# Optimization experiments

Measured on AMD Instinct MI355X. Metric: run time of the kernel, lower is better.

The kernel has to match this reference:

```python
import jax, jax.numpy as jnp
import numpy as np

MAX_JOINTS = 143

def setup_inputs() -> dict:
    key = jax.random.key(0)
    ks = jax.random.split(key, 8)
    d_model, latent_dim, feat = 256, 512, 13
    s = lambda n: 1.0 / np.sqrt(n)
    return {
        "z": jax.random.normal(ks[0], (32, latent_dim), jnp.float32),
        "W_latent": jax.random.normal(ks[1], (latent_dim, d_model), jnp.float32) * s(latent_dim),
        "b_latent": jnp.zeros((d_model,), jnp.float32),
        "joint_emb": jax.random.normal(ks[2], (MAX_JOINTS, d_model), jnp.float32),
        "frame_emb": jax.random.normal(ks[3], (120, d_model), jnp.float32),
        "ln_gamma": jnp.ones((d_model,), jnp.float32),
        "ln_beta": jnp.zeros((d_model,), jnp.float32),
        "W1": jax.random.normal(ks[4], (d_model, d_model), jnp.float32) * s(d_model),
        "b1": jnp.zeros((d_model,), jnp.float32),
        "W2": jax.random.normal(ks[5], (d_model, feat), jnp.float32) * s(d_model),
        "b2": jnp.zeros((feat,), jnp.float32),
        "max_frames": 120,
    }

def reference(z, W_latent, b_latent, joint_emb, frame_emb, ln_gamma, ln_beta, W1, b1, W2, b2, max_frames):
    # base: [B, d]
    base = z @ W_latent + b_latent
    fe = frame_emb[:max_frames]  # [F, d]
    # three-way broadcast sum -> [B, J, F, d]
    hidden = base[:, None, None, :] + joint_emb[None, :, None, :] + fe[None, None, :, :]
    # LayerNorm over last dim (eps=1e-5, torch default)
    mu = jnp.mean(hidden, axis=-1, keepdims=True)
    var = jnp.mean(jnp.square(hidden - mu), axis=-1, keepdims=True)
    h = (hidden - mu) * jax.lax.rsqrt(var + 1e-5) * ln_gamma + ln_beta
    # MLP: Linear -> exact GELU -> Linear
    h = jax.nn.gelu(h @ W1 + b1, approximate=False)
    out = h @ W2 + b2  # [B, J, F, feat]
    return jnp.transpose(out, (0, 1, 3, 2))  # [B, J, feat, F]
```

## Files before the change

kernel.cpp:

```cpp
#include <hip/hip_runtime.h>
#include <hip/hip_bf16.h>

typedef __bf16 bf16x8 __attribute__((ext_vector_type(8)));
typedef float  f32x4  __attribute__((ext_vector_type(4)));
typedef float  f32x2  __attribute__((ext_vector_type(2)));

#define B_  32
#define J_  143
#define F_  120
#define D_  256
#define L_  512
#define C_  13
#define M_  4576
#define NK  256
#define QB  9
#define GRIDC 509
#define CLS 260
#define PXS 388

static __device__ __forceinline__ unsigned short bits(__bf16 h) {
  return __builtin_bit_cast(unsigned short, h);
}

__global__ __launch_bounds__(256) void prep_kernel(
    const float* __restrict__ z, const float* __restrict__ Wl,
    const float* __restrict__ bl, const float* __restrict__ W1,
    const float* __restrict__ gamma, const float* __restrict__ beta,
    const float* __restrict__ b1, const float* __restrict__ fe,
    const float* __restrict__ W2,
    float* __restrict__ base, unsigned short* __restrict__ BT,
    float* __restrict__ bW1, float* __restrict__ Sfe, float* __restrict__ Sfe2,
    unsigned short* __restrict__ W2T, float* __restrict__ P2f) {
  const int t = threadIdx.x, bid = blockIdx.x;
  const int lane = t & 63, wv = t >> 6;
  __shared__ float zs[L_];
  __shared__ float ra[4], rb[4];
  __shared__ float fegl[256], gl2[256];

  if (bid < 32) {
    zs[t]       = z[bid * L_ + t];
    zs[t + 256] = z[bid * L_ + t + 256];
    __syncthreads();
    float acc = 0.f;
    #pragma unroll 32
    for (int k = 0; k < L_; ++k) acc = __builtin_fmaf(zs[k], Wl[k * D_ + t], acc);
    base[bid * D_ + t] = acc + bl[t];
    return;
  }
  if (bid < 432) {
    const int n = bid - 32;
    if (n < 256) {
      const float w1v = W1[t * D_ + n];
      float a = gamma[t] * w1v;
      float b = beta[t] * w1v;
      const float wg = a;
      #pragma unroll
      for (int m = 1; m < 64; m <<= 1) { a += __shfl_xor(a, m); b += __shfl_xor(b, m); }
      if (lane == 0) { ra[wv] = a; rb[wv] = b; }
      __syncthreads();
      const float cs = ra[0] + ra[1] + ra[2] + ra[3];
      if (t == 0) bW1[n] = rb[0] + rb[1] + rb[2] + rb[3] + b1[n];
      const float m = __builtin_fmaf(cs, -1.f / 256.f, wg);
      BT[n * NK + t] = bits((__bf16)m);
    } else if (n < 376) {
      const int f = n - 256;
      const float v = fe[f * D_ + t];
      float a = v, b = v * v;
      #pragma unroll
      for (int m = 1; m < 64; m <<= 1) { a += __shfl_xor(a, m); b += __shfl_xor(b, m); }
      if (lane == 0) { ra[wv] = a; rb[wv] = b; }
      __syncthreads();
      if (t == 0) {
        Sfe[f]  = ra[0] + ra[1] + ra[2] + ra[3];
        Sfe2[f] = rb[0] + rb[1] + rb[2] + rb[3];
      }
      BT[n * NK + t] = bits((__bf16)v);
    } else if (n < 384) {
      BT[n * NK + t] = 0;
    } else {
      const int c = n - 384;
      const float v = (c < C_) ? W2[t * C_ + c] : 0.f;
      W2T[c * D_ + t] = bits((__bf16)v);
    }
    return;
  }
  {
    const int f = bid - 432;
    const float fv = fe[f * D_ + t];
    const float gv = gamma[t];
    fegl[t] = fv * gv;
    gl2[t]  = gv;
    float a = fv;
    #pragma unroll
    for (int m = 1; m < 64; m <<= 1) a += __shfl_xor(a, m);
    if (lane == 0) ra[wv] = a;
    __syncthreads();
    const float sfe = ra[0] + ra[1] + ra[2] + ra[3];
    float acc1 = 0.f, acc2 = 0.f;
    #pragma unroll 8
    for (int k = 0; k < 256; ++k) {
      const float w = W1[k * D_ + t];
      acc1 = __builtin_fmaf(fegl[k], w, acc1);
      acc2 = __builtin_fmaf(gl2[k],  w, acc2);
    }
    P2f[f * D_ + t] = __builtin_fmaf(-sfe * (1.f / 256.f), acc2, acc1);
  }
}

__global__ __launch_bounds__(512, 4) void megaC_kernel(
    const float* __restrict__ base, const float* __restrict__ joint,
    const unsigned short* __restrict__ BT, const float* __restrict__ P2f,
    const float* __restrict__ bW1,
    const float* __restrict__ Sfe, const float* __restrict__ Sfe2,
    const unsigned short* __restrict__ W2T, const float* __restrict__ b2,
    float* __restrict__ out) {
  __shared__ float cl[16 * CLS];
  __shared__ float px[QB * PXS];
  __shared__ float bw[256];
  __shared__ float rstdl[QB][128];
  __shared__ float Scl[QB], Sc2l[QB];
  __shared__ __align__(16) unsigned short w2l[4096];

  const int tid  = threadIdx.x;
  const int lane = tid & 63, wv = tid >> 6;
  const int lrow = lane & 15, lgrp = lane >> 4;
  const int bj0  = blockIdx.x * QB;

  #pragma unroll
  for (int i = 0; i < 8; ++i) {
    const int idx = tid + i * 512;
    const int row = idx >> 8, col = idx & 255;
    float v = 0.f;
    if (row < QB) {
      const int bj = min(bj0 + row, M_ - 1);
      const int b = bj / J_, j = bj - b * J_;
      v = base[b * D_ + col] + joint[j * D_ + col];
    }
    cl[row * CLS + col] = v;
  }
  if (tid < 256) {
    bw[tid] = bW1[tid];
    const int rr = tid >> 4;
    const int b0 = tid * 32;
    const int sb = b0 ^ ((rr & 7) << 4);
    *(uint4*)((char*)w2l + sb)        = *(const uint4*)((const char*)W2T + b0);
    *(uint4*)((char*)w2l + (sb ^ 16)) = *(const uint4*)((const char*)W2T + b0 + 16);
  }
  __syncthreads();

  for (int r = wv; r < QB; r += 8) {
    const float4 v4 = *(const float4*)(cl + r * CLS + lane * 4);
    float s = v4.x + v4.y + v4.z + v4.w;
    float q = __builtin_fmaf(v4.x, v4.x,
              __builtin_fmaf(v4.y, v4.y,
              __builtin_fmaf(v4.z, v4.z, v4.w * v4.w)));
    #pragma unroll
    for (int m = 1; m < 64; m <<= 1) { s += __shfl_xor(s, m); q += __shfl_xor(q, m); }
    if (lane == 0) { Scl[r] = s; Sc2l[r] = q; }
  }

  {
    const int colbase = wv * 48;
    f32x4 acc[3] = {};
    #pragma unroll
    for (int s8 = 0; s8 < 8; ++s8) {
      const int k0 = s8 * 32 + lgrp * 8;
      const float4 c0 = *(const float4*)(cl + lrow * CLS + k0);
      const float4 c1 = *(const float4*)(cl + lrow * CLS + k0 + 4);
      const float cc[8] = {c0.x, c0.y, c0.z, c0.w, c1.x, c1.y, c1.z, c1.w};
      bf16x8 ahi;
      #pragma unroll
      for (int e = 0; e < 8; ++e) ahi[e] = (__bf16)cc[e];
      bf16x8 bhi[3];
      #pragma unroll
      for (int cf = 0; cf < 3; ++cf)
        bhi[cf] = *(const bf16x8*)(BT + (size_t)(colbase + cf * 16 + lrow) * NK +
                                   lgrp * 8 + s8 * 32);
      #pragma unroll
      for (int cf = 0; cf < 3; ++cf)
        acc[cf] = __builtin_amdgcn_mfma_f32_16x16x32_bf16(ahi, bhi[cf], acc[cf], 0, 0, 0);
    }
    #pragma unroll
    for (int cf = 0; cf < 3; ++cf)
      #pragma unroll
      for (int r4 = 0; r4 < 4; ++r4) {
        const int row = lgrp * 4 + r4;
        if (row < QB)
          px[row * PXS + colbase + cf * 16 + lrow] = acc[cf][r4];
      }
  }
  __syncthreads();

  #pragma unroll
  for (int i = 0; i < 3; ++i) {
    const int id2 = tid + i * 512;
    if (id2 < QB * 128) {
      const int q = id2 >> 7;
      const int fr = id2 & 127;
      const int fc = fr < F_ ? fr : F_ - 1;
      const float X = px[q * PXS + 256 + fc];
      const float mu = (Scl[q] + Sfe[fc]) * (1.f / 256.f);
      const float ms = __builtin_fmaf(2.f, X, Sc2l[q] + Sfe2[fc]) * (1.f / 256.f);
      rstdl[q][fr] = rsqrtf(ms - mu * mu + 1e-5f);
    }
  }
  __syncthreads();

  const int r0 = wv * 16 + lrow;
  const int f0 = r0 < F_ ? r0 : F_ - 1;
  float rs[QB];
  #pragma unroll
  for (int q = 0; q < QB; ++q) rs[q] = rstdl[q][r0];
  const float* __restrict__ q0p = P2f + f0 * D_ + lgrp * 8;

  f32x4 acc2[QB] = {};
  #pragma unroll
  for (int s = 0; s < 8; ++s) {
    const int n0 = s * 32 + lgrp * 8;
    const float4 qa0 = *(const float4*)(q0p + s * 32);
    const float4 qa1 = *(const float4*)(q0p + s * 32 + 4);
    const bf16x8 w2f = *(const bf16x8*)((const char*)w2l +
        ((lrow * 512 + n0 * 2) ^ ((lrow & 7) << 4)));
    f32x2 QV[4], BV[4];
    QV[0].x = qa0.x; QV[0].y = qa0.y;
    QV[1].x = qa0.z; QV[1].y = qa0.w;
    QV[2].x = qa1.x; QV[2].y = qa1.y;
    QV[3].x = qa1.z; QV[3].y = qa1.w;
    #pragma unroll
    for (int ep = 0; ep < 4; ++ep) BV[ep] = *(const f32x2*)(&bw[n0 + 2 * ep]);

    #pragma unroll
    for (int g = 0; g < QB; g += 3) {
      f32x2 U[12];
      #pragma unroll
      for (int qq = 0; qq < 3; ++qq) {
        f32x2 RS; RS.x = rs[g + qq]; RS.y = rs[g + qq];
        #pragma unroll
        for (int ep = 0; ep < 4; ++ep) {
          const f32x2 P = *(const f32x2*)(&px[(g + qq) * PXS + n0 + 2 * ep]);
          U[qq * 4 + ep] = __builtin_elementwise_fma(RS, P + QV[ep], BV[ep]);
        }
      }
      f32x2 E[12];
      #pragma unroll
      for (int i = 0; i < 12; ++i) {
        const f32x2 u = U[i];
        const f32x2 x2 = u * u;
        const f32x2 tt = u * (x2 * -0.1029432f + -2.3022082f);
        E[i].x = __builtin_amdgcn_exp2f(tt.x);
        E[i].y = __builtin_amdgcn_exp2f(tt.y);
      }
      bf16x8 af[3];
      #pragma unroll
      for (int i = 0; i < 12; ++i) {
        const f32x2 d = E[i] + 1.0f;
        f32x2 r;
        r.x = __builtin_amdgcn_rcpf(d.x);
        r.y = __builtin_amdgcn_rcpf(d.y);
        const f32x2 G = U[i] * r;
        af[i >> 2][(i & 3) * 2]     = (__bf16)G.x;
        af[i >> 2][(i & 3) * 2 + 1] = (__bf16)G.y;
      }
      #pragma unroll
      for (int qq = 0; qq < 3; ++qq)
        acc2[g + qq] =
            __builtin_amdgcn_mfma_f32_16x16x32_bf16(af[qq], w2f, acc2[g + qq], 0, 0, 0);
    }
  }

  if (lrow < C_) {
    const float bias = b2[lrow];
    const int f = wv * 16 + lgrp * 4;
    if (f < F_) {
      #pragma unroll
      for (int q = 0; q < QB; ++q) {
        if (bj0 + q < M_) {
          float4 v;
          v.x = acc2[q][0] + bias;
          v.y = acc2[q][1] + bias;
          v.z = acc2[q][2] + bias;
          v.w = acc2[q][3] + bias;
          *(float4*)(out + (size_t)(bj0 + q) * (C_ * F_) + lrow * F_ + f) = v;
        }
      }
    }
  }
}

extern "C" void kernel_launch(void* const* d_in, const int* in_sizes, int n_in,
                              void* d_out, int out_size, void* d_ws, size_t ws_size,
                              hipStream_t stream) {
  const float* z     = (const float*)d_in[0];
  const float* Wl    = (const float*)d_in[1];
  const float* bl    = (const float*)d_in[2];
  const float* joint = (const float*)d_in[3];
  const float* fe    = (const float*)d_in[4];
  const float* gamma = (const float*)d_in[5];
  const float* beta  = (const float*)d_in[6];
  const float* W1    = (const float*)d_in[7];
  const float* b1    = (const float*)d_in[8];
  const float* W2    = (const float*)d_in[9];
  const float* b2    = (const float*)d_in[10];
  float* out = (float*)d_out;

  char* ws = (char*)d_ws;
  float*          base  = (float*)(ws + 0);
  unsigned short* W2T   = (unsigned short*)(ws + 32768);
  float*          bW1   = (float*)(ws + 40960);
  float*          Sfe   = (float*)(ws + 41984);
  float*          Sfe2  = (float*)(ws + 42496);
  float*          P2f   = (float*)(ws + 65536);
  unsigned short* BT    = (unsigned short*)(ws + 262144);

  prep_kernel<<<552, 256, 0, stream>>>(z, Wl, bl, W1, gamma, beta, b1, fe, W2,
                                       base, BT, bW1, Sfe, Sfe2, W2T, P2f);
  megaC_kernel<<<GRIDC, 512, 0, stream>>>(base, joint, BT, P2f, bW1,
                                          Sfe, Sfe2, W2T, b2, out);
}
```

Measured before the change: 69.00 us.

## Split fused kernel into standalone bf16 GEMM pass plus smaller-tile MLP kernel

Moves the first projection (base+joint rows times BT) and the per-row sum and sum-of-squares out of the main kernel into a separate tiled MFMA GEMM kernel that writes an intermediate PXg buffer to workspace. The main kernel then loads precomputed rows, processes 6 rows per block instead of 9 with higher occupancy (launch bounds 512,6), and no longer pays for redundant 16-row MFMA tiles where only 9 rows are used. This trades an extra launch and a global round-trip of the intermediate for better compute utilisation and occupancy. A runtime check on spill bytes falls back to the old fused kernel.

```diff
diff --git a/kernel.cpp b/kernel.cpp
--- a/kernel.cpp
+++ b/kernel.cpp
@@ -12,11 +12,11 @@
 #define L_  512
 #define C_  13
 #define M_  4576
+#define MPAD 4736
 #define NK  256
-#define QB  9
-#define GRIDC 509
 #define CLS 260
 #define PXS 388
+#define PXG 384
 
 static __device__ __forceinline__ unsigned short bits(__bf16 h) {
   return __builtin_bit_cast(unsigned short, h);
@@ -107,36 +107,91 @@
   }
 }
 
-__global__ __launch_bounds__(512, 4) void megaC_kernel(
+__global__ __launch_bounds__(256, 4) void gemmBk_kernel(
     const float* __restrict__ base, const float* __restrict__ joint,
-    const unsigned short* __restrict__ BT, const float* __restrict__ P2f,
+    const unsigned short* __restrict__ BT,
+    float* __restrict__ PXg, float* __restrict__ Sc, float* __restrict__ Sc2) {
+  const int tid = threadIdx.x, lane = tid & 63, wave = tid >> 6;
+  const int lrow = lane & 15, lgrp = lane >> 4;
+  const int rb_ = blockIdx.x / 6, cb_ = blockIdx.x % 6;
+  const int rowbase = rb_ * 64 + wave * 16;
+  const int colbase = cb_ * 64;
+  const int r = rowbase + lrow;
+  const int bj = min(r, M_ - 1);
+  const int b = bj / J_, j = bj - b * J_;
+  const float* p1 = base + b * D_;
+  const float* p2 = joint + j * D_;
+
+  f32x4 acc[4] = {};
+  float ssum = 0.f, ssq = 0.f;
+  #pragma unroll
+  for (int s8 = 0; s8 < 8; ++s8) {
+    const int k0 = s8 * 32 + lgrp * 8;
+    const float4 ca = *(const float4*)(p1 + k0);
+    const float4 cb4 = *(const float4*)(p1 + k0 + 4);
+    const float4 da = *(const float4*)(p2 + k0);
+    const float4 db = *(const float4*)(p2 + k0 + 4);
+    const float c[8] = {ca.x + da.x, ca.y + da.y, ca.z + da.z, ca.w + da.w,
+                        cb4.x + db.x, cb4.y + db.y, cb4.z + db.z, cb4.w + db.w};
+    bf16x8 ahi;
+    #pragma unroll
+    for (int e = 0; e < 8; ++e) ahi[e] = (__bf16)c[e];
+    if (cb_ == 0) {
+      #pragma unroll
+      for (int e = 0; e < 8; ++e) { ssum += c[e]; ssq = __builtin_fmaf(c[e], c[e], ssq); }
+    }
+    bf16x8 bhi[4];
+    #pragma unroll
+    for (int nf = 0; nf < 4; ++nf)
+      bhi[nf] = *(const bf16x8*)(BT + (size_t)(colbase + nf * 16 + lrow) * NK +
+                                 lgrp * 8 + s8 * 32);
+    #pragma unroll
+    for (int nf = 0; nf < 4; ++nf)
+      acc[nf] = __builtin_amdgcn_mfma_f32_16x16x32_bf16(ahi, bhi[nf], acc[nf], 0, 0, 0);
+  }
+
+  if (cb_ == 0) {
+    ssum += __shfl_xor(ssum, 16); ssum += __shfl_xor(ssum, 32);
+    ssq  += __shfl_xor(ssq, 16);  ssq  += __shfl_xor(ssq, 32);
+    if (lgrp == 0 && r < M_) { Sc[r] = ssum; Sc2[r] = ssq; }
+  }
+
+  #pragma unroll
+  for (int nf = 0; nf < 4; ++nf)
+    #pragma unroll
+    for (int r4 = 0; r4 < 4; ++r4)
+      PXg[(size_t)(rowbase + lgrp * 4 + r4) * PXG + colbase + nf * 16 + lrow] =
+          acc[nf][r4];
+}
+
+#define QB2 6
+#define GRIDC2 763
+__global__ __launch_bounds__(512, 6) void mainC2_kernel(
+    const float* __restrict__ PXg, const float* __restrict__ P2f,
     const float* __restrict__ bW1,
+    const float* __restrict__ Sc, const float* __restrict__ Sc2,
     const float* __restrict__ Sfe, const float* __restrict__ Sfe2,
     const unsigned short* __restrict__ W2T, const float* __restrict__ b2,
     float* __restrict__ out) {
-  __shared__ float cl[16 * CLS];
-  __shared__ float px[QB * PXS];
+  __shared__ float pxl[QB2 * PXS];
   __shared__ float bw[256];
-  __shared__ float rstdl[QB][128];
-  __shared__ float Scl[QB], Sc2l[QB];
+  __shared__ float rstdl[QB2][128];
+  __shared__ float Scl[QB2], Sc2l[QB2];
   __shared__ __align__(16) unsigned short w2l[4096];
 
   const int tid  = threadIdx.x;
   const int lane = tid & 63, wv = tid >> 6;
   const int lrow = lane & 15, lgrp = lane >> 4;
-  const int bj0  = blockIdx.x * QB;
-
-  #pragma unroll
-  for (int i = 0; i < 8; ++i) {
+  const int bj0  = blockIdx.x * QB2;
+
+  #pragma unroll
+  for (int i = 0; i < 5; ++i) {
     const int idx = tid + i * 512;
-    const int row = idx >> 8, col = idx & 255;
-    float v = 0.f;
-    if (row < QB) {
-      const int bj = min(bj0 + row, M_ - 1);
-      const int b = bj / J_, j = bj - b * J_;
-      v = base[b * D_ + col] + joint[j * D_ + col];
-    }
-    cl[row * CLS + col] = v;
+    if (idx < QB2 * PXG) {
+      const int q = idx / PXG;
+      const int n = idx - q * PXG;
+      pxl[q * PXS + n] = PXg[(size_t)(bj0 + q) * PXG + n];
+    }
   }
   if (tid < 256) {
     bw[tid] = bW1[tid];
@@ -146,59 +201,21 @@
     *(uint4*)((char*)w2l + sb)        = *(const uint4*)((const char*)W2T + b0);
     *(uint4*)((char*)w2l + (sb ^ 16)) = *(const uint4*)((const char*)W2T + b0 + 16);
   }
+  if (tid < QB2) {
+    const int bj = min(bj0 + tid, M_ - 1);
+    Scl[tid] = Sc[bj];
+    Sc2l[tid] = Sc2[bj];
+  }
   __syncthreads();
 
-  for (int r = wv; r < QB; r += 8) {
-    const float4 v4 = *(const float4*)(cl + r * CLS + lane * 4);
-    float s = v4.x + v4.y + v4.z + v4.w;
-    float q = __builtin_fmaf(v4.x, v4.x,
-              __builtin_fmaf(v4.y, v4.y,
-              __builtin_fmaf(v4.z, v4.z, v4.w * v4.w)));
-    #pragma unroll
-    for (int m = 1; m < 64; m <<= 1) { s += __shfl_xor(s, m); q += __shfl_xor(q, m); }
-    if (lane == 0) { Scl[r] = s; Sc2l[r] = q; }
-  }
-
-  {
-    const int colbase = wv * 48;
-    f32x4 acc[3] = {};
-    #pragma unroll
-    for (int s8 = 0; s8 < 8; ++s8) {
-      const int k0 = s8 * 32 + lgrp * 8;
-      const float4 c0 = *(const float4*)(cl + lrow * CLS + k0);
-      const float4 c1 = *(const float4*)(cl + lrow * CLS + k0 + 4);
-      const float cc[8] = {c0.x, c0.y, c0.z, c0.w, c1.x, c1.y, c1.z, c1.w};
-      bf16x8 ahi;
-      #pragma unroll
-      for (int e = 0; e < 8; ++e) ahi[e] = (__bf16)cc[e];
-      bf16x8 bhi[3];
-      #pragma unroll
-      for (int cf = 0; cf < 3; ++cf)
-        bhi[cf] = *(const bf16x8*)(BT + (size_t)(colbase + cf * 16 + lrow) * NK +
-                                   lgrp * 8 + s8 * 32);
-      #pragma unroll
-      for (int cf = 0; cf < 3; ++cf)
-        acc[cf] = __builtin_amdgcn_mfma_f32_16x16x32_bf16(ahi, bhi[cf], acc[cf], 0, 0, 0);
-    }
-    #pragma unroll
-    for (int cf = 0; cf < 3; ++cf)
-      #pragma unroll
-      for (int r4 = 0; r4 < 4; ++r4) {
-        const int row = lgrp * 4 + r4;
-        if (row < QB)
-          px[row * PXS + colbase + cf * 16 + lrow] = acc[cf][r4];
-      }
-  }
-  __syncthreads();
-
-  #pragma unroll
-  for (int i = 0; i < 3; ++i) {
+  #pragma unroll
+  for (int i = 0; i < 2; ++i) {
     const int id2 = tid + i * 512;
-    if (id2 < QB * 128) {
+    if (id2 < QB2 * 128) {
       const int q = id2 >> 7;
       const int fr = id2 & 127;
       const int fc = fr < F_ ? fr : F_ - 1;
-      const float X = px[q * PXS + 256 + fc];
+      const float X = pxl[q * PXS + 256 + fc];
       const float mu = (Scl[q] + Sfe[fc]) * (1.f / 256.f);
       const float ms = __builtin_fmaf(2.f, X, Sc2l[q] + Sfe2[fc]) * (1.f / 256.f);
       rstdl[q][fr] = rsqrtf(ms - mu * mu + 1e-5f);
@@ -208,12 +225,12 @@
 
   const int r0 = wv * 16 + lrow;
   const int f0 = r0 < F_ ? r0 : F_ - 1;
-  float rs[QB];
-  #pragma unroll
-  for (int q = 0; q < QB; ++q) rs[q] = rstdl[q][r0];
+  float rs[QB2];
+  #pragma unroll
+  for (int q = 0; q < QB2; ++q) rs[q] = rstdl[q][r0];
   const float* __restrict__ q0p = P2f + f0 * D_ + lgrp * 8;
 
-  f32x4 acc2[QB] = {};
+  f32x4 acc2[QB2] = {};
   #pragma unroll
   for (int s = 0; s < 8; ++s) {
     const int n0 = s * 32 + lgrp * 8;
@@ -230,7 +247,183 @@
     for (int ep = 0; ep < 4; ++ep) BV[ep] = *(const f32x2*)(&bw[n0 + 2 * ep]);
 
     #pragma unroll
-    for (int g = 0; g < QB; g += 3) {
+    for (int q = 0; q < QB2; ++q) {
+      f32x2 RS; RS.x = rs[q]; RS.y = rs[q];
+      f32x2 U[4];
+      #pragma unroll
+      for (int ep = 0; ep < 4; ++ep) {
+        const f32x2 P = *(const f32x2*)(&pxl[q * PXS + n0 + 2 * ep]);
+        U[ep] = __builtin_elementwise_fma(RS, P + QV[ep], BV[ep]);
+      }
+      f32x2 E[4];
+      #pragma unroll
+      for (int i = 0; i < 4; ++i) {
+        const f32x2 u = U[i];
+        const f32x2 x2 = u * u;
+        const f32x2 tt = u * (x2 * -0.1029432f + -2.3022082f);
+        E[i].x = __builtin_amdgcn_exp2f(tt.x);
+        E[i].y = __builtin_amdgcn_exp2f(tt.y);
+      }
+      bf16x8 af;
+      #pragma unroll
+      for (int i = 0; i < 4; ++i) {
+        const f32x2 d = E[i] + 1.0f;
+        f32x2 r;
+        r.x = __builtin_amdgcn_rcpf(d.x);
+        r.y = __builtin_amdgcn_rcpf(d.y);
+        const f32x2 G = U[i] * r;
+        af[i * 2]     = (__bf16)G.x;
+        af[i * 2 + 1] = (__bf16)G.y;
+      }
+      acc2[q] = __builtin_amdgcn_mfma_f32_16x16x32_bf16(af, w2f, acc2[q], 0, 0, 0);
+    }
+  }
+
+  if (lrow < C_) {
+    const float bias = b2[lrow];
+    const int f = wv * 16 + lgrp * 4;
+    if (f < F_) {
+      #pragma unroll
+      for (int q = 0; q < QB2; ++q) {
+        if (bj0 + q < M_) {
+          float4 v;
+          v.x = acc2[q][0] + bias;
+          v.y = acc2[q][1] + bias;
+          v.z = acc2[q][2] + bias;
+          v.w = acc2[q][3] + bias;
+          *(float4*)(out + (size_t)(bj0 + q) * (C_ * F_) + lrow * F_ + f) = v;
+        }
+      }
+    }
+  }
+}
+
+#define QB9 9
+#define GRIDC9 509
+__global__ __launch_bounds__(512, 4) void megaC_kernel(
+    const float* __restrict__ base, const float* __restrict__ joint,
+    const unsigned short* __restrict__ BT, const float* __restrict__ P2f,
+    const float* __restrict__ bW1,
+    const float* __restrict__ Sfe, const float* __restrict__ Sfe2,
+    const unsigned short* __restrict__ W2T, const float* __restrict__ b2,
+    float* __restrict__ out) {
+  __shared__ float cl[16 * CLS];
+  __shared__ float px[QB9 * PXS];
+  __shared__ float bw[256];
+  __shared__ float rstdl[QB9][128];
+  __shared__ float Scl[QB9], Sc2l[QB9];
+  __shared__ __align__(16) unsigned short w2l[4096];
+
+  const int tid  = threadIdx.x;
+  const int lane = tid & 63, wv = tid >> 6;
+  const int lrow = lane & 15, lgrp = lane >> 4;
+  const int bj0  = blockIdx.x * QB9;
+
+  #pragma unroll
+  for (int i = 0; i < 8; ++i) {
+    const int idx = tid + i * 512;
+    const int row = idx >> 8, col = idx & 255;
+    float v = 0.f;
+    if (row < QB9) {
+      const int bj = min(bj0 + row, M_ - 1);
+      const int b = bj / J_, j = bj - b * J_;
+      v = base[b * D_ + col] + joint[j * D_ + col];
+    }
+    cl[row * CLS + col] = v;
+  }
+  if (tid < 256) {
+    bw[tid] = bW1[tid];
+    const int rr = tid >> 4;
+    const int b0 = tid * 32;
+    const int sb = b0 ^ ((rr & 7) << 4);
+    *(uint4*)((char*)w2l + sb)        = *(const uint4*)((const char*)W2T + b0);
+    *(uint4*)((char*)w2l + (sb ^ 16)) = *(const uint4*)((const char*)W2T + b0 + 16);
+  }
+  __syncthreads();
+
+  for (int r = wv; r < QB9; r += 8) {
+    const float4 v4 = *(const float4*)(cl + r * CLS + lane * 4);
+    float s = v4.x + v4.y + v4.z + v4.w;
+    float q = __builtin_fmaf(v4.x, v4.x,
+              __builtin_fmaf(v4.y, v4.y,
+              __builtin_fmaf(v4.z, v4.z, v4.w * v4.w)));
+    #pragma unroll
+    for (int m = 1; m < 64; m <<= 1) { s += __shfl_xor(s, m); q += __shfl_xor(q, m); }
+    if (lane == 0) { Scl[r] = s; Sc2l[r] = q; }
+  }
+
+  {
+    const int colbase = wv * 48;
+    f32x4 acc[3] = {};
+    #pragma unroll
+    for (int s8 = 0; s8 < 8; ++s8) {
+      const int k0 = s8 * 32 + lgrp * 8;
+      const float4 c0 = *(const float4*)(cl + lrow * CLS + k0);
+      const float4 c1 = *(const float4*)(cl + lrow * CLS + k0 + 4);
+      const float cc[8] = {c0.x, c0.y, c0.z, c0.w, c1.x, c1.y, c1.z, c1.w};
+      bf16x8 ahi;
+      #pragma unroll
+      for (int e = 0; e < 8; ++e) ahi[e] = (__bf16)cc[e];
+      bf16x8 bhi[3];
+      #pragma unroll
+      for (int cf = 0; cf < 3; ++cf)
+        bhi[cf] = *(const bf16x8*)(BT + (size_t)(colbase + cf * 16 + lrow) * NK +
+                                   lgrp * 8 + s8 * 32);
+      #pragma unroll
+      for (int cf = 0; cf < 3; ++cf)
+        acc[cf] = __builtin_amdgcn_mfma_f32_16x16x32_bf16(ahi, bhi[cf], acc[cf], 0, 0, 0);
+    }
+    #pragma unroll
+    for (int cf = 0; cf < 3; ++cf)
+      #pragma unroll
+      for (int r4 = 0; r4 < 4; ++r4) {
+        const int row = lgrp * 4 + r4;
+        if (row < QB9)
+          px[row * PXS + colbase + cf * 16 + lrow] = acc[cf][r4];
+      }
+  }
+  __syncthreads();
+
+  #pragma unroll
+  for (int i = 0; i < 3; ++i) {
+    const int id2 = tid + i * 512;
+    if (id2 < QB9 * 128) {
+      const int q = id2 >> 7;
+      const int fr = id2 & 127;
+      const int fc = fr < F_ ? fr : F_ - 1;
+      const float X = px[q * PXS + 256 + fc];
+      const float mu = (Scl[q] + Sfe[fc]) * (1.f / 256.f);
+      const float ms = __builtin_fmaf(2.f, X, Sc2l[q] + Sfe2[fc]) * (1.f / 256.f);
+      rstdl[q][fr] = rsqrtf(ms - mu * mu + 1e-5f);
+    }
+  }
+  __syncthreads();
+
+  const int r0 = wv * 16 + lrow;
+  const int f0 = r0 < F_ ? r0 : F_ - 1;
+  float rs[QB9];
+  #pragma unroll
+  for (int q = 0; q < QB9; ++q) rs[q] = rstdl[q][r0];
+  const float* __restrict__ q0p = P2f + f0 * D_ + lgrp * 8;
+
+  f32x4 acc2[QB9] = {};
+  #pragma unroll
+  for (int s = 0; s < 8; ++s) {
+    const int n0 = s * 32 + lgrp * 8;
+    const float4 qa0 = *(const float4*)(q0p + s * 32);
+    const float4 qa1 = *(const float4*)(q0p + s * 32 + 4);
+    const bf16x8 w2f = *(const bf16x8*)((const char*)w2l +
+        ((lrow * 512 + n0 * 2) ^ ((lrow & 7) << 4)));
+    f32x2 QV[4], BV[4];
+    QV[0].x = qa0.x; QV[0].y = qa0.y;
+    QV[1].x = qa0.z; QV[1].y = qa0.w;
+    QV[2].x = qa1.x; QV[2].y = qa1.y;
+    QV[3].x = qa1.z; QV[3].y = qa1.w;
+    #pragma unroll
+    for (int ep = 0; ep < 4; ++ep) BV[ep] = *(const f32x2*)(&bw[n0 + 2 * ep]);
+
+    #pragma unroll
+    for (int g = 0; g < QB9; g += 3) {
       f32x2 U[12];
       #pragma unroll
       for (int qq = 0; qq < 3; ++qq) {
@@ -273,7 +466,7 @@
     const int f = wv * 16 + lgrp * 4;
     if (f < F_) {
       #pragma unroll
-      for (int q = 0; q < QB; ++q) {
+      for (int q = 0; q < QB9; ++q) {
         if (bj0 + q < M_) {
           float4 v;
           v.x = acc2[q][0] + bias;
@@ -309,11 +502,25 @@
   float*          bW1   = (float*)(ws + 40960);
   float*          Sfe   = (float*)(ws + 41984);
   float*          Sfe2  = (float*)(ws + 42496);
-  float*          P2f   = (float*)(ws + 65536);
+  float*          Sc    = (float*)(ws + 49152);
+  float*          Sc2   = (float*)(ws + 69632);
+  float*          P2f   = (float*)(ws + 98304);
   unsigned short* BT    = (unsigned short*)(ws + 262144);
+  float*          PXg   = (float*)(ws + 524288);
 
   prep_kernel<<<552, 256, 0, stream>>>(z, Wl, bl, W1, gamma, beta, b1, fe, W2,
                                        base, BT, bW1, Sfe, Sfe2, W2T, P2f);
-  megaC_kernel<<<GRIDC, 512, 0, stream>>>(base, joint, BT, P2f, bW1,
-                                          Sfe, Sfe2, W2T, b2, out);
+
+  hipFuncAttributes a{};
+  const bool ok = (hipFuncGetAttributes(&a, (const void*)mainC2_kernel) == hipSuccess) &&
+                  (a.localSizeBytes == 0);
+
+  if (ok) {
+    gemmBk_kernel<<<444, 256, 0, stream>>>(base, joint, BT, PXg, Sc, Sc2);
+    mainC2_kernel<<<GRIDC2, 512, 0, stream>>>(PXg, P2f, bW1, Sc, Sc2, Sfe, Sfe2,
+                                              W2T, b2, out);
+  } else {
+    megaC_kernel<<<GRIDC9, 512, 0, stream>>>(base, joint, BT, P2f, bW1,
+                                             Sfe, Sfe2, W2T, b2, out);
+  }
 }
```

New measurement: 76.14 us. 10.3% more time.
